# Optimization experiments

Measured on AMD Instinct MI355X. Metric: run time of the kernel, lower is better.

The kernel has to match this reference:

```python
import jax, jax.numpy as jnp
import numpy as np

NPOINT = 1024   # number of sampled centers
NSAMPLE = 32    # neighbors per center
BN_EPS = 1e-5


def setup_inputs() -> dict:
    key = jax.random.key(0)
    ks = jax.random.split(key, 6)
    B, N, C = 8, 4096, 6
    inp = {
        "xyz": jax.random.normal(ks[0], (B, N, 3), jnp.float32),
        "points": jax.random.normal(ks[1], (B, N, C), jnp.float32),
        "W0": jax.random.normal(ks[2], (64, 9), jnp.float32) * 0.1,
        "g0": jnp.ones((64,), jnp.float32),
        "b0": jnp.zeros((64,), jnp.float32),
        "W1": jax.random.normal(ks[3], (64, 64), jnp.float32) * 0.1,
        "g1": jnp.ones((64,), jnp.float32),
        "b1": jnp.zeros((64,), jnp.float32),
        "W2": jax.random.normal(ks[4], (128, 64), jnp.float32) * 0.1,
        "g2": jnp.ones((128,), jnp.float32),
        "b2": jnp.zeros((128,), jnp.float32),
    }
    return inp


def sample_and_group(xyz, points):
    # xyz: [B,N,3], points: [B,N,C]
    B, N, _ = xyz.shape
    stride = N // NPOINT
    new_xyz = xyz[:, ::stride]                      # [B,S,3] deterministic subsample (FPS surrogate)
    # squared pairwise distances via ||a||^2 + ||b||^2 - 2 a.b  -> [B,S,N]
    d = (jnp.sum(new_xyz * new_xyz, -1)[:, :, None]
         + jnp.sum(xyz * xyz, -1)[:, None, :]
         - 2.0 * jnp.einsum('bsd,bnd->bsn', new_xyz, xyz))
    _, idx = jax.lax.top_k(-d, NSAMPLE)             # [B,S,K] KNN indices
    gather = jax.vmap(lambda arr, i: arr[i])        # per-batch gather: [N,C],[S,K] -> [S,K,C]
    g_xyz = gather(xyz, idx) - new_xyz[:, :, None, :]   # relative coords [B,S,K,3]
    g_pts = gather(points, idx)                     # [B,S,K,C]
    new_points = jnp.concatenate([g_xyz, g_pts], -1)    # [B,S,K,3+C]
    return new_xyz, new_points


def mlp_layer(x, W, g, b):
    # Conv2d(1x1, bias=False) == channel contraction; BN2d with batch stats; ReLU
    x = jnp.einsum('bskc,oc->bsko', x, W)
    m = jnp.mean(x, axis=(0, 1, 2))
    v = jnp.var(x, axis=(0, 1, 2))
    x = (x - m) * jax.lax.rsqrt(v + BN_EPS) * g + b
    return jax.nn.relu(x)


def reference(xyz, points, W0, g0, b0, W1, g1, b1, W2, g2, b2):
    new_xyz, x = sample_and_group(xyz, points)      # x: [B,S,K,9]
    x = mlp_layer(x, W0, g0, b0)
    x = mlp_layer(x, W1, g1, b1)
    x = mlp_layer(x, W2, g2, b2)
    new_points = jnp.max(x, axis=2)                 # max-pool over neighbor dim K -> [B,S,128]
    return new_xyz, new_points
```

## Files before the change

### kernel.cpp

```cpp
#include <hip/hip_runtime.h>
#include <float.h>
#include <stdint.h>

#define TOT   262144
#define NPTS  4096
#define KNN   32
#define BN_EPS 1e-5f
#define CAPV  64

typedef _Float16 f16;
typedef _Float16 f16x2 __attribute__((ext_vector_type(2)));
typedef _Float16 f16x4 __attribute__((ext_vector_type(4)));
typedef _Float16 f16x8 __attribute__((ext_vector_type(8)));
typedef float    f32x4 __attribute__((ext_vector_type(4)));

__device__ __forceinline__ int mbcnt64(unsigned long long m){
  return __builtin_amdgcn_mbcnt_hi((unsigned)(m>>32),
         __builtin_amdgcn_mbcnt_lo((unsigned)(m & 0xffffffffull), 0));
}
__device__ __forceinline__ unsigned f2ord(float f){
  unsigned u = __float_as_uint(f);
  return u ^ (((unsigned)((int)u >> 31)) | 0x80000000u);
}
__device__ __forceinline__ f16x2 bnrelu2(f16x2 x, f16x2 a, f16x2 c){
  f16x2 r = x*a + c;
  const f16 z = (f16)0.f;
  r[0] = r[0] > z ? r[0] : z;
  r[1] = r[1] > z ? r[1] : z;
  return r;
}
__device__ __forceinline__ void writeElem(int n, int e, float qx, float qy, float qz,
    const float4* __restrict__ xb, const float* __restrict__ fb,
    f16* __restrict__ grouped, f16* __restrict__ g16){
  float4 P = xb[n];
  f16 a[16];
  a[0]=(f16)(P.x-qx); a[1]=(f16)(P.y-qy); a[2]=(f16)(P.z-qz);
  #pragma unroll
  for (int c6=0;c6<6;c6++) a[3+c6] = (f16)fb[n*6+c6];
  #pragma unroll
  for (int i=9;i<16;i++) a[i]=(f16)0.f;
  #pragma unroll
  for (int c=0;c<9;c++) grouped[c*TOT+e] = a[c];
  f16x8 lo, hi;
  #pragma unroll
  for (int i=0;i<8;i++){ lo[i]=a[i]; hi[i]=a[8+i]; }
  *(f16x8*)(g16 + (size_t)e*16)     = lo;
  *(f16x8*)(g16 + (size_t)e*16 + 8) = hi;
}

__global__ __launch_bounds__(256) void prep(const float* __restrict__ xyz,
    float4* __restrict__ xyzp){
  int p = blockIdx.x*256 + threadIdx.x;
  float x = xyz[p*3+0], y = xyz[p*3+1], z = xyz[p*3+2];
  xyzp[p] = make_float4(x, y, z, x*x+y*y+z*z);
}

__global__ __launch_bounds__(256) void knn_gather(
    const float4* __restrict__ xyzp, const float* __restrict__ pts,
    f16* __restrict__ grouped, f16* __restrict__ g16,
    float* __restrict__ out_newxyz){
  __shared__ unsigned wkbuf[4][4][CAPV];
  __shared__ unsigned short wibuf[4][4][CAPV];
  __shared__ unsigned lcnt[4][4];
  const int lane = threadIdx.x & 63;
  const int wv   = threadIdx.x >> 6;
  const int q0 = (blockIdx.x*4 + wv)*4;
  const int b = q0 >> 10, s0 = q0 & 1023;
  const float4* xb = xyzp + b*NPTS;
  float qx[4], qy[4], qz[4], qq[4];
  #pragma unroll
  for (int t=0;t<4;t++){
    float4 Q = xb[(s0+t)*4];
    qx[t]=Q.x; qy[t]=Q.y; qz[t]=Q.z; qq[t]=Q.w;
  }
  if (lane < 4) lcnt[wv][lane] = 0;
  if (lane == 0){
    #pragma unroll
    for (int t=0;t<4;t++){
      out_newxyz[(q0+t)*3+0]=qx[t]; out_newxyz[(q0+t)*3+1]=qy[t];
      out_newxyz[(q0+t)*3+2]=qz[t];
    }
  }

  unsigned mm[4] = {0xFFFFFFFFu,0xFFFFFFFFu,0xFFFFFFFFu,0xFFFFFFFFu};
  #pragma unroll 4
  for (int j=0;j<64;j++){
    float4 P = xb[j*64+lane];
    #pragma unroll
    for (int t=0;t<4;t++){
      float d = (qq[t]+P.w) - 2.f*(qx[t]*P.x+qy[t]*P.y+qz[t]*P.z);
      unsigned k = f2ord(d);
      mm[t] = k<mm[t] ? k : mm[t];
    }
  }
  unsigned sm[4] = {mm[0],mm[1],mm[2],mm[3]};
  #pragma unroll
  for (int k=2;k<=64;k<<=1){
    #pragma unroll
    for (int j=k>>1;j>0;j>>=1){
      bool keepmin = (((lane&k)==0) == ((lane&j)==0));
      #pragma unroll
      for (int t=0;t<4;t++){
        unsigned o = __shfl_xor(sm[t], j, 64);
        sm[t] = keepmin ? (sm[t]<o?sm[t]:o) : (sm[t]>o?sm[t]:o);
      }
    }
  }
  unsigned U[4];
  #pragma unroll
  for (int t=0;t<4;t++) U[t] = __shfl(sm[t], 31, 64);

  #pragma unroll 2
  for (int j=0;j<64;j++){
    float4 P = xb[j*64+lane];
    #pragma unroll
    for (int t=0;t<4;t++){
      float d = (qq[t]+P.w) - 2.f*(qx[t]*P.x+qy[t]*P.y+qz[t]*P.z);
      unsigned k = f2ord(d);
      if (k <= U[t]){
        unsigned p = atomicAdd(&lcnt[wv][t], 1u);
        if (p < CAPV){ wkbuf[wv][t][p]=k; wibuf[wv][t][p]=(unsigned short)(j*64+lane); }
      }
    }
  }
  int cnt[4];
  #pragma unroll
  for (int t=0;t<4;t++) cnt[t] = (int)lcnt[wv][t];

  unsigned long long v[4];
  #pragma unroll
  for (int t=0;t<4;t++){
    unsigned myk = (lane<cnt[t]) ? wkbuf[wv][t][lane] : 0xFFFFFFFFu;
    unsigned myi = (lane<cnt[t]) ? wibuf[wv][t][lane] : 0u;
    v[t] = (((unsigned long long)myk)<<16) | myi;
  }
  #pragma unroll
  for (int k=2;k<=64;k<<=1){
    #pragma unroll
    for (int j=k>>1;j>0;j>>=1){
      bool keepmin = (((lane&k)==0) == ((lane&j)==0));
      #pragma unroll
      for (int t=0;t<4;t++){
        unsigned long long o = __shfl_xor(v[t], j, 64);
        v[t] = keepmin ? (v[t]<o?v[t]:o) : (v[t]>o?v[t]:o);
      }
    }
  }

  const float* fb = pts + (size_t)b*NPTS*6;
  #pragma unroll
  for (int t=0;t<4;t++){
    const int ebase = (q0+t)*KNN;
    if (cnt[t] <= CAPV){
      if (lane < KNN){
        int n = (int)(v[t] & 0xffffull);
        writeElem(n, ebase+lane, qx[t],qy[t],qz[t], xb, fb, grouped, g16);
      }
    } else {
      unsigned V=0;
      for (int bit=31; bit>=0; --bit){
        unsigned X = V | (1u<<bit);
        int c=0;
        for (int j=0;j<64;j++){
          float4 P = xb[j*64+lane];
          float d = (qq[t]+P.w) - 2.f*(qx[t]*P.x+qy[t]*P.y+qz[t]*P.z);
          c += __popcll(__ballot(f2ord(d) < X));
        }
        if (c < KNN) V = X;
      }
      int cnt2=0;
      for (int pass=0; pass<2; ++pass){
        for (int j=0;j<64;j++){
          float4 P = xb[j*64+lane];
          float d = (qq[t]+P.w) - 2.f*(qx[t]*P.x+qy[t]*P.y+qz[t]*P.z);
          unsigned kk = f2ord(d);
          bool sel = pass ? (kk==V) : (kk<V);
          unsigned long long msk = __ballot(sel);
          int pos = cnt2 + mbcnt64(msk);
          if (sel && pos < KNN)
            writeElem(j*64+lane, ebase+pos, qx[t],qy[t],qz[t], xb, fb, grouped, g16);
          cnt2 += __popcll(msk);
        }
      }
    }
  }
}

__global__ __launch_bounds__(256) void stats0m(const f16* __restrict__ grouped,
    float* __restrict__ s0m){
  const int lane = threadIdx.x & 63, wv = threadIdx.x >> 6;
  const int c = lane & 15, q = lane >> 4;
  const int base = (blockIdx.x*4 + wv)*512;
  f16x8 cfill = {};
  if (c == 9){
    #pragma unroll
    for (int i=0;i<8;i++) cfill[i] = (f16)1.f;
  }
  f32x4 acc = {0.f,0.f,0.f,0.f};
  #pragma unroll 4
  for (int chunk=0; chunk<16; ++chunk){
    int e = base + chunk*32 + q*8;
    f16x8 f = cfill;
    if (c < 9) f = *(const f16x8*)(grouped + (size_t)c*TOT + e);
    acc = __builtin_amdgcn_mfma_f32_16x16x32_f16(f, f, acc, 0,0,0);
  }
  __shared__ float red[4][16][16];
  #pragma unroll
  for (int i=0;i<4;i++) red[wv][q*4+i][c] = acc[i];
  __syncthreads();
  const int tid = threadIdx.x;
  if (tid < 160){
    int row = tid>>4, col = tid&15;
    float vv = red[0][row][col]+red[1][row][col]+red[2][row][col]+red[3][row][col];
    atomicAdd(&s0m[tid], vv);
  }
}

__global__ void finalize0(const float* __restrict__ s0m,
    const float* __restrict__ W0, const float* __restrict__ g0,
    const float* __restrict__ b0, float* __restrict__ ac0,
    const float* __restrict__ W1, const float* __restrict__ W2,
    f16* __restrict__ W0h, f16* __restrict__ W1h, f16* __restrict__ W2h){
  const int tid = threadIdx.x;
  __shared__ float S[160];
  __shared__ float A0s[64];
  if (tid < 160) S[tid] = s0m[tid];
  __syncthreads();
  if (tid < 64){
    float w[9];
    #pragma unroll
    for (int c=0;c<9;c++) w[c]=W0[tid*9+c];
    const float inv = 1.f/(float)TOT;
    float m=0.f;
    #pragma unroll
    for (int c=0;c<9;c++) m = fmaf(w[c], S[c*16+9], m);
    m *= inv;
    float e2=0.f;
    #pragma unroll
    for (int c1=0;c1<9;c1++){
      float t=0.f;
      #pragma unroll
      for (int c2=0;c2<9;c2++) t = fmaf(w[c2], S[c1*16+c2], t);
      e2 = fmaf(w[c1], t, e2);
    }
    e2 *= inv;
    float var = e2 - m*m;
    float a = g0[tid]*rsqrtf(var + BN_EPS);
    ac0[tid]    = a;
    ac0[64+tid] = fmaf(-m, a, b0[tid]);
    A0s[tid]    = a;
  }
  __syncthreads();
  for (int i=tid; i<2048; i+=256){
    int o = i>>5, c = i&31;
    W0h[i] = (f16)(c<9 ? A0s[o]*W0[o*9+c] : 0.f);
  }
  for (int i=tid; i<4096; i+=256) W1h[i] = (f16)W1[i];
  for (int i=tid; i<8192; i+=256) W2h[i] = (f16)W2[i];
}

__global__ __launch_bounds__(256) void layer1s(
    const f16* __restrict__ g16, const f16* __restrict__ W0h,
    const f16* __restrict__ W1h, const float* __restrict__ ac0,
    float* __restrict__ s1g){
  __shared__ f16 sW0[2048];
  __shared__ f16 sW1[4096];
  __shared__ float ac0c[64];
  __shared__ f16 hb0[4][16][72];
  __shared__ float sred[4][128];
  const int tid = threadIdx.x;
  const int lane = tid & 63, wv = tid >> 6;
  const int e16 = lane & 15, q = lane >> 4;
  *(f16x8*)(&sW0[tid*8]) = *(const f16x8*)(W0h + tid*8);
  *(f16x8*)(&sW1[tid*8])        = *(const f16x8*)(W1h + tid*8);
  *(f16x8*)(&sW1[2048 + tid*8]) = *(const f16x8*)(W1h + 2048 + tid*8);
  if (tid < 64) ac0c[tid] = ac0[64+tid];
  __syncthreads();

  const int base = blockIdx.x*512 + wv*128;
  float ssum[16], ssq[16];
  #pragma unroll
  for (int i=0;i<16;i++){ ssum[i]=0.f; ssq[i]=0.f; }

  #pragma unroll 1
  for (int sub=0; sub<8; ++sub){
    int elem = base + sub*16 + e16;
    f16x8 bg = {};
    if (q < 2) bg = *(const f16x8*)(g16 + (size_t)elem*16 + q*8);
    #pragma unroll
    for (int m=0;m<4;m++){
      f32x4 acc = *(const f32x4*)(&ac0c[m*16 + q*4]);
      f16x8 A0f = *(const f16x8*)(&sW0[(m*16+e16)*32 + q*8]);
      acc = __builtin_amdgcn_mfma_f32_16x16x32_f16(A0f, bg, acc, 0,0,0);
      f16x4 w;
      w[0]=(f16)fmaxf(acc[0],0.f); w[1]=(f16)fmaxf(acc[1],0.f);
      w[2]=(f16)fmaxf(acc[2],0.f); w[3]=(f16)fmaxf(acc[3],0.f);
      *(f16x4*)(&hb0[wv][e16][m*16 + q*4]) = w;
    }
    f32x4 acc2[4];
    #pragma unroll
    for (int m=0;m<4;m++) acc2[m] = (f32x4){0.f,0.f,0.f,0.f};
    #pragma unroll
    for (int s=0;s<2;s++){
      f16x8 bh = *(const f16x8*)(&hb0[wv][e16][s*32 + q*8]);
      #pragma unroll
      for (int m=0;m<4;m++){
        f16x8 A1f = *(const f16x8*)(&sW1[(m*16+e16)*64 + s*32 + q*8]);
        acc2[m] = __builtin_amdgcn_mfma_f32_16x16x32_f16(A1f, bh, acc2[m], 0,0,0);
      }
    }
    #pragma unroll
    for (int m=0;m<4;m++)
      #pragma unroll
      for (int i=0;i<4;i++){
        float x = acc2[m][i];
        ssum[m*4+i] += x;
        ssq[m*4+i]  = fmaf(x, x, ssq[m*4+i]);
      }
  }
  #pragma unroll
  for (int t=0;t<16;t++){
    float a = ssum[t], bq = ssq[t];
    #pragma unroll
    for (int off=1; off<16; off<<=1){
      a  += __shfl_xor(a,  off, 64);
      bq += __shfl_xor(bq, off, 64);
    }
    ssum[t]=a; ssq[t]=bq;
  }
  if (e16==0){
    #pragma unroll
    for (int m=0;m<4;m++)
      #pragma unroll
      for (int i=0;i<4;i++){
        int ch = m*16 + q*4 + i;
        sred[wv][ch]    = ssum[m*4+i];
        sred[wv][64+ch] = ssq[m*4+i];
      }
  }
  __syncthreads();
  if (tid < 128){
    float v = sred[0][tid]+sred[1][tid]+sred[2][tid]+sred[3][tid];
    atomicAdd(&s1g[tid], v);
  }
}

__global__ __launch_bounds__(256) void layer2max(
    const f16* __restrict__ g16, const f16* __restrict__ W0h,
    const f16* __restrict__ W1h, const f16* __restrict__ W2h,
    const float* __restrict__ ac0, const float* __restrict__ s1g,
    const float* __restrict__ g1, const float* __restrict__ b1,
    float* __restrict__ maxbuf, float* __restrict__ s2g){
  __shared__ f16 sW0[2048];
  __shared__ f16 sW1[4096];
  __shared__ float ac0c[64];
  __shared__ f16 ac1s[128];
  __shared__ f16 hb0[4][16][72];
  __shared__ f16 hb1[4][2][16][72];
  __shared__ float lds[4][256];
  const int tid = threadIdx.x;
  const int lane = tid & 63, wv = tid >> 6;
  const int e16 = lane & 15, q = lane >> 4;
  *(f16x8*)(&sW0[tid*8]) = *(const f16x8*)(W0h + tid*8);
  *(f16x8*)(&sW1[tid*8])        = *(const f16x8*)(W1h + tid*8);
  *(f16x8*)(&sW1[2048 + tid*8]) = *(const f16x8*)(W1h + 2048 + tid*8);
  if (tid < 64) ac0c[tid] = ac0[64+tid];
  if (tid < 64){
    const float inv = 1.f/(float)TOT;
    float m = s1g[tid]*inv;
    float vv = s1g[64+tid]*inv - m*m;
    float a = g1[tid]*rsqrtf(vv + BN_EPS);
    ac1s[tid]    = (f16)a;
    ac1s[64+tid] = (f16)fmaf(-m, a, b1[tid]);
  }
  __syncthreads();

  f16x8 Bw[8][2];
  #pragma unroll
  for (int nt=0;nt<8;nt++)
    #pragma unroll
    for (int s=0;s<2;s++) Bw[nt][s] = *(const f16x8*)(W2h + (nt*16+e16)*64 + s*32 + q*8);

  float ssum[8], ssq[8];
  #pragma unroll
  for (int i=0;i<8;i++){ ssum[i]=0.f; ssq[i]=0.f; }

  #pragma unroll 1
  for (int qq=0; qq<4; ++qq){
    const int qid = blockIdx.x*16 + wv*4 + qq;
    #pragma unroll 1
    for (int mt=0; mt<2; ++mt){
      int elem = qid*32 + mt*16 + e16;
      f16x8 bg = {};
      if (q < 2) bg = *(const f16x8*)(g16 + (size_t)elem*16 + q*8);
      #pragma unroll
      for (int m=0;m<4;m++){
        f32x4 acc = *(const f32x4*)(&ac0c[m*16 + q*4]);
        f16x8 A0f = *(const f16x8*)(&sW0[(m*16+e16)*32 + q*8]);
        acc = __builtin_amdgcn_mfma_f32_16x16x32_f16(A0f, bg, acc, 0,0,0);
        f16x4 w;
        w[0]=(f16)fmaxf(acc[0],0.f); w[1]=(f16)fmaxf(acc[1],0.f);
        w[2]=(f16)fmaxf(acc[2],0.f); w[3]=(f16)fmaxf(acc[3],0.f);
        *(f16x4*)(&hb0[wv][e16][m*16 + q*4]) = w;
      }
      f32x4 acc2[4];
      #pragma unroll
      for (int m=0;m<4;m++) acc2[m] = (f32x4){0.f,0.f,0.f,0.f};
      #pragma unroll
      for (int s=0;s<2;s++){
        f16x8 bh = *(const f16x8*)(&hb0[wv][e16][s*32 + q*8]);
        #pragma unroll
        for (int m=0;m<4;m++){
          f16x8 A1f = *(const f16x8*)(&sW1[(m*16+e16)*64 + s*32 + q*8]);
          acc2[m] = __builtin_amdgcn_mfma_f32_16x16x32_f16(A1f, bh, acc2[m], 0,0,0);
        }
      }
      #pragma unroll
      for (int m=0;m<4;m++){
        f16x4 a4 = *(const f16x4*)(&ac1s[m*16 + q*4]);
        f16x4 c4 = *(const f16x4*)(&ac1s[64 + m*16 + q*4]);
        f16x2 p0 = bnrelu2((f16x2){(f16)acc2[m][0], (f16)acc2[m][1]},
                           (f16x2){a4[0],a4[1]}, (f16x2){c4[0],c4[1]});
        f16x2 p1 = bnrelu2((f16x2){(f16)acc2[m][2], (f16)acc2[m][3]},
                           (f16x2){a4[2],a4[3]}, (f16x2){c4[2],c4[3]});
        f16x4 w; w[0]=p0[0]; w[1]=p0[1]; w[2]=p1[0]; w[3]=p1[1];
        *(f16x4*)(&hb1[wv][mt][e16][m*16 + q*4]) = w;
      }
    }
    float mx[8];
    #pragma unroll 1
    for (int g=0; g<2; ++g){
      f32x4 acc3[4][2];
      #pragma unroll
      for (int j=0;j<4;j++){ acc3[j][0]=(f32x4){0,0,0,0}; acc3[j][1]=(f32x4){0,0,0,0}; }
      #pragma unroll
      for (int mt=0; mt<2; ++mt)
        #pragma unroll
        for (int s=0;s<2;s++){
          f16x8 af = *(const f16x8*)(&hb1[wv][mt][e16][s*32 + q*8]);
          #pragma unroll
          for (int j=0;j<4;j++)
            acc3[j][mt] = __builtin_amdgcn_mfma_f32_16x16x32_f16(af, Bw[g*4+j][s], acc3[j][mt], 0,0,0);
        }
      #pragma unroll
      for (int j=0;j<4;j++){
        int nt = g*4 + j;
        f32x4 u = acc3[j][0], vv = acc3[j][1];
        float m1 = fmaxf(fmaxf(u[0],u[1]), fmaxf(u[2],u[3]));
        float m2 = fmaxf(fmaxf(vv[0],vv[1]), fmaxf(vv[2],vv[3]));
        float m = fmaxf(m1, m2);
        ssum[nt] += (u[0]+u[1])+(u[2]+u[3]) + (vv[0]+vv[1])+(vv[2]+vv[3]);
        float sq = 0.f;
        #pragma unroll
        for (int i=0;i<4;i++){ sq = fmaf(u[i],u[i],sq); sq = fmaf(vv[i],vv[i],sq); }
        ssq[nt] += sq;
        m = fmaxf(m, __shfl_xor(m, 16, 64));
        m = fmaxf(m, __shfl_xor(m, 32, 64));
        mx[nt] = m;
      }
    }
    if (lane < 16){
      #pragma unroll
      for (int nt=0;nt<8;nt++) maxbuf[(size_t)qid*128 + nt*16 + lane] = mx[nt];
    }
  }
  #pragma unroll
  for (int nt=0;nt<8;nt++){
    ssum[nt] += __shfl_xor(ssum[nt], 16, 64);
    ssum[nt] += __shfl_xor(ssum[nt], 32, 64);
    ssq[nt]  += __shfl_xor(ssq[nt], 16, 64);
    ssq[nt]  += __shfl_xor(ssq[nt], 32, 64);
  }
  if (q==0){
    #pragma unroll
    for (int nt=0;nt<8;nt++){
      lds[wv][nt*16+e16]     = ssum[nt];
      lds[wv][128+nt*16+e16] = ssq[nt];
    }
  }
  __syncthreads();
  float v = lds[0][tid]+lds[1][tid]+lds[2][tid]+lds[3][tid];
  atomicAdd(&s2g[tid], v);
}

__global__ __launch_bounds__(256) void apply2(
    const float* __restrict__ maxbuf, const float* __restrict__ s2g,
    const float* __restrict__ g2, const float* __restrict__ b2,
    float* __restrict__ outp){
  __shared__ float a2s[128], c2s[128];
  const int tid = threadIdx.x;
  if (tid < 128){
    const float inv = 1.f/(float)TOT;
    float m = s2g[tid]*inv;
    float v = s2g[128+tid]*inv - m*m;
    float a = g2[tid]*rsqrtf(v + BN_EPS);
    a2s[tid] = a;
    c2s[tid] = fmaf(-m, a, b2[tid]);
  }
  __syncthreads();
  int i = blockIdx.x*256 + tid;
  int o = i & 127;
  outp[i] = fmaxf(fmaf(maxbuf[i], a2s[o], c2s[o]), 0.f);
}

extern "C" void kernel_launch(void* const* d_in, const int* in_sizes, int n_in,
                              void* d_out, int out_size, void* d_ws, size_t ws_size,
                              hipStream_t stream){
  const float* xyz = (const float*)d_in[0];
  const float* pts = (const float*)d_in[1];
  const float* W0  = (const float*)d_in[2];
  const float* g0  = (const float*)d_in[3];
  const float* b0  = (const float*)d_in[4];
  const float* W1  = (const float*)d_in[5];
  const float* g1  = (const float*)d_in[6];
  const float* b1  = (const float*)d_in[7];
  const float* W2  = (const float*)d_in[8];
  const float* g2  = (const float*)d_in[9];
  const float* b2  = (const float*)d_in[10];
  float* out = (float*)d_out;

  float* ws      = (float*)d_ws;
  f16*   grouped = (f16*)ws;
  f16*   g16     = (f16*)(ws + (size_t)5*TOT);
  float* maxbuf  = ws + (size_t)13*TOT;
  float4* xyzp   = (float4*)(ws + (size_t)17*TOT);
  float* basep   = ws + (size_t)17*TOT + 131072;
  f16*   W0h     = (f16*)basep;
  f16*   W1h     = (f16*)(basep + 1024);
  f16*   W2h     = (f16*)(basep + 3072);
  float* s0m     = basep + 7168;
  float* s1g     = s0m + 160;
  float* s2g     = s1g + 128;
  float* ac0     = s2g + 256;

  (void)hipMemsetAsync(s0m, 0, 544*sizeof(float), stream);
  prep      <<< 128, 256, 0, stream>>>(xyz, xyzp);
  knn_gather<<< 512, 256, 0, stream>>>(xyzp, pts, grouped, g16, out);
  stats0m   <<< 128, 256, 0, stream>>>(grouped, s0m);
  finalize0 <<<   1, 256, 0, stream>>>(s0m, W0, g0, b0, ac0, W1, W2, W0h, W1h, W2h);
  layer1s   <<< 512, 256, 0, stream>>>(g16, W0h, W1h, ac0, s1g);
  layer2max <<< 512, 256, 0, stream>>>(g16, W0h, W1h, W2h, ac0, s1g, g1, b1, maxbuf, s2g);
  apply2    <<<4096, 256, 0, stream>>>(maxbuf, s2g, g2, b2, out + 24576);
}
```

Baseline: 207.3 us.

## Stage KNN point cloud in LDS tiles, halve queries per wave, double grid sizes

The KNN kernel now loads the batch's points cooperatively into a shared-memory tile of 1024 float4s and has each wave read from it. Each wave now handles two queries instead of four, and the distance thresholding compares floats instead of order-mapped integers. The KNN, layer1s and layer2max grids are doubled to 1024 blocks with half the work per block, for more parallelism and occupancy. The cost is extra block barriers, the tile reloaded per block, and less reuse of each loaded point across queries.

```diff
diff --git a/kernel.cpp b/kernel.cpp
--- a/kernel.cpp
+++ b/kernel.cpp
@@ -59,79 +59,93 @@
     const float4* __restrict__ xyzp, const float* __restrict__ pts,
     f16* __restrict__ grouped, f16* __restrict__ g16,
     float* __restrict__ out_newxyz){
-  __shared__ unsigned wkbuf[4][4][CAPV];
-  __shared__ unsigned short wibuf[4][4][CAPV];
-  __shared__ unsigned lcnt[4][4];
-  const int lane = threadIdx.x & 63;
-  const int wv   = threadIdx.x >> 6;
-  const int q0 = (blockIdx.x*4 + wv)*4;
-  const int b = q0 >> 10, s0 = q0 & 1023;
+  __shared__ float4 tile[1024];
+  __shared__ unsigned wk[8][CAPV];
+  __shared__ unsigned short wi[8][CAPV];
+  __shared__ unsigned lcnt[8];
+  const int tid = threadIdx.x, lane = tid & 63, wv = tid >> 6;
+  const int q0 = blockIdx.x*8 + wv*2;
+  const int b  = (blockIdx.x*8) >> 10;
   const float4* xb = xyzp + b*NPTS;
-  float qx[4], qy[4], qz[4], qq[4];
-  #pragma unroll
-  for (int t=0;t<4;t++){
-    float4 Q = xb[(s0+t)*4];
+  float qx[2],qy[2],qz[2],qq[2];
+  #pragma unroll
+  for (int t=0;t<2;t++){
+    int s = (q0+t) & 1023;
+    float4 Q = xb[s*4];
     qx[t]=Q.x; qy[t]=Q.y; qz[t]=Q.z; qq[t]=Q.w;
   }
-  if (lane < 4) lcnt[wv][lane] = 0;
+  if (tid < 8) lcnt[tid] = 0;
   if (lane == 0){
     #pragma unroll
-    for (int t=0;t<4;t++){
+    for (int t=0;t<2;t++){
       out_newxyz[(q0+t)*3+0]=qx[t]; out_newxyz[(q0+t)*3+1]=qy[t];
       out_newxyz[(q0+t)*3+2]=qz[t];
     }
   }
 
-  unsigned mm[4] = {0xFFFFFFFFu,0xFFFFFFFFu,0xFFFFFFFFu,0xFFFFFFFFu};
-  #pragma unroll 4
-  for (int j=0;j<64;j++){
-    float4 P = xb[j*64+lane];
-    #pragma unroll
-    for (int t=0;t<4;t++){
-      float d = (qq[t]+P.w) - 2.f*(qx[t]*P.x+qy[t]*P.y+qz[t]*P.z);
-      unsigned k = f2ord(d);
-      mm[t] = k<mm[t] ? k : mm[t];
-    }
-  }
-  unsigned sm[4] = {mm[0],mm[1],mm[2],mm[3]};
+  float dmin[2] = {FLT_MAX, FLT_MAX};
+  #pragma unroll 1
+  for (int tl=0; tl<4; ++tl){
+    __syncthreads();
+    #pragma unroll
+    for (int i=0;i<4;i++) tile[i*256+tid] = xb[tl*1024 + i*256 + tid];
+    __syncthreads();
+    #pragma unroll 4
+    for (int i=0;i<16;i++){
+      float4 P = tile[i*64+lane];
+      #pragma unroll
+      for (int t=0;t<2;t++){
+        float d = (qq[t]+P.w) - 2.f*(qx[t]*P.x+qy[t]*P.y+qz[t]*P.z);
+        dmin[t] = d < dmin[t] ? d : dmin[t];
+      }
+    }
+  }
+  float sm[2] = {dmin[0], dmin[1]};
   #pragma unroll
   for (int k=2;k<=64;k<<=1){
     #pragma unroll
     for (int j=k>>1;j>0;j>>=1){
       bool keepmin = (((lane&k)==0) == ((lane&j)==0));
       #pragma unroll
-      for (int t=0;t<4;t++){
-        unsigned o = __shfl_xor(sm[t], j, 64);
-        sm[t] = keepmin ? (sm[t]<o?sm[t]:o) : (sm[t]>o?sm[t]:o);
-      }
-    }
-  }
-  unsigned U[4];
-  #pragma unroll
-  for (int t=0;t<4;t++) U[t] = __shfl(sm[t], 31, 64);
-
-  #pragma unroll 2
-  for (int j=0;j<64;j++){
-    float4 P = xb[j*64+lane];
-    #pragma unroll
-    for (int t=0;t<4;t++){
-      float d = (qq[t]+P.w) - 2.f*(qx[t]*P.x+qy[t]*P.y+qz[t]*P.z);
-      unsigned k = f2ord(d);
-      if (k <= U[t]){
-        unsigned p = atomicAdd(&lcnt[wv][t], 1u);
-        if (p < CAPV){ wkbuf[wv][t][p]=k; wibuf[wv][t][p]=(unsigned short)(j*64+lane); }
-      }
-    }
-  }
-  int cnt[4];
-  #pragma unroll
-  for (int t=0;t<4;t++) cnt[t] = (int)lcnt[wv][t];
-
-  unsigned long long v[4];
-  #pragma unroll
-  for (int t=0;t<4;t++){
-    unsigned myk = (lane<cnt[t]) ? wkbuf[wv][t][lane] : 0xFFFFFFFFu;
-    unsigned myi = (lane<cnt[t]) ? wibuf[wv][t][lane] : 0u;
+      for (int t=0;t<2;t++){
+        float o = __shfl_xor(sm[t], j, 64);
+        sm[t] = keepmin ? fminf(sm[t],o) : fmaxf(sm[t],o);
+      }
+    }
+  }
+  float Uf[2];
+  #pragma unroll
+  for (int t=0;t<2;t++) Uf[t] = __shfl(sm[t], 31, 64);
+
+  #pragma unroll 1
+  for (int tl=0; tl<4; ++tl){
+    __syncthreads();
+    #pragma unroll
+    for (int i=0;i<4;i++) tile[i*256+tid] = xb[tl*1024 + i*256 + tid];
+    __syncthreads();
+    #pragma unroll 2
+    for (int i=0;i<16;i++){
+      float4 P = tile[i*64+lane];
+      #pragma unroll
+      for (int t=0;t<2;t++){
+        float d = (qq[t]+P.w) - 2.f*(qx[t]*P.x+qy[t]*P.y+qz[t]*P.z);
+        if (d <= Uf[t]){
+          unsigned p = atomicAdd(&lcnt[wv*2+t], 1u);
+          if (p < CAPV){
+            wk[wv*2+t][p] = f2ord(d);
+            wi[wv*2+t][p] = (unsigned short)(tl*1024 + i*64 + lane);
+          }
+        }
+      }
+    }
+  }
+  int cnt[2] = {(int)lcnt[wv*2], (int)lcnt[wv*2+1]};
+
+  unsigned long long v[2];
+  #pragma unroll
+  for (int t=0;t<2;t++){
+    unsigned myk = (lane<cnt[t]) ? wk[wv*2+t][lane] : 0xFFFFFFFFu;
+    unsigned myi = (lane<cnt[t]) ? wi[wv*2+t][lane] : 0u;
     v[t] = (((unsigned long long)myk)<<16) | myi;
   }
   #pragma unroll
@@ -140,7 +154,7 @@
     for (int j=k>>1;j>0;j>>=1){
       bool keepmin = (((lane&k)==0) == ((lane&j)==0));
       #pragma unroll
-      for (int t=0;t<4;t++){
+      for (int t=0;t<2;t++){
         unsigned long long o = __shfl_xor(v[t], j, 64);
         v[t] = keepmin ? (v[t]<o?v[t]:o) : (v[t]>o?v[t]:o);
       }
@@ -148,8 +162,8 @@
   }
 
   const float* fb = pts + (size_t)b*NPTS*6;
-  #pragma unroll
-  for (int t=0;t<4;t++){
+  #pragma unroll 1
+  for (int t=0;t<2;t++){
     const int ebase = (q0+t)*KNN;
     if (cnt[t] <= CAPV){
       if (lane < KNN){
@@ -277,13 +291,13 @@
   if (tid < 64) ac0c[tid] = ac0[64+tid];
   __syncthreads();
 
-  const int base = blockIdx.x*512 + wv*128;
+  const int base = blockIdx.x*256 + wv*64;
   float ssum[16], ssq[16];
   #pragma unroll
   for (int i=0;i<16;i++){ ssum[i]=0.f; ssq[i]=0.f; }
 
   #pragma unroll 1
-  for (int sub=0; sub<8; ++sub){
+  for (int sub=0; sub<4; ++sub){
     int elem = base + sub*16 + e16;
     f16x8 bg = {};
     if (q < 2) bg = *(const f16x8*)(g16 + (size_t)elem*16 + q*8);
@@ -386,8 +400,8 @@
   for (int i=0;i<8;i++){ ssum[i]=0.f; ssq[i]=0.f; }
 
   #pragma unroll 1
-  for (int qq=0; qq<4; ++qq){
-    const int qid = blockIdx.x*16 + wv*4 + qq;
+  for (int qq=0; qq<2; ++qq){
+    const int qid = blockIdx.x*8 + wv*2 + qq;
     #pragma unroll 1
     for (int mt=0; mt<2; ++mt){
       int elem = qid*32 + mt*16 + e16;
@@ -535,10 +549,10 @@
 
   (void)hipMemsetAsync(s0m, 0, 544*sizeof(float), stream);
   prep      <<< 128, 256, 0, stream>>>(xyz, xyzp);
-  knn_gather<<< 512, 256, 0, stream>>>(xyzp, pts, grouped, g16, out);
+  knn_gather<<<1024, 256, 0, stream>>>(xyzp, pts, grouped, g16, out);
   stats0m   <<< 128, 256, 0, stream>>>(grouped, s0m);
   finalize0 <<<   1, 256, 0, stream>>>(s0m, W0, g0, b0, ac0, W1, W2, W0h, W1h, W2h);
-  layer1s   <<< 512, 256, 0, stream>>>(g16, W0h, W1h, ac0, s1g);
-  layer2max <<< 512, 256, 0, stream>>>(g16, W0h, W1h, W2h, ac0, s1g, g1, b1, maxbuf, s2g);
+  layer1s   <<<1024, 256, 0, stream>>>(g16, W0h, W1h, ac0, s1g);
+  layer2max <<<1024, 256, 0, stream>>>(g16, W0h, W1h, W2h, ac0, s1g, g1, b1, maxbuf, s2g);
   apply2    <<<4096, 256, 0, stream>>>(maxbuf, s2g, g2, b2, out + 24576);
 }
```

Measured after the change: 217.2 us. +4.8%, slower.
